# Optimization experiments

Measured on AMD Instinct MI355X. Metric: run time of the kernel, lower is better.

The kernel has to match this reference:

```python
import jax, jax.numpy as jnp
import numpy as np

N = 20000
E = 320000
NEG_SLOPE = 0.2
LN_EPS = 1e-5


def gat_conv(x, W, a_src, a_dst, b, src, dst, heads, ch, concat):
    # x: [N, F_in]; W: [F_in, H*C]; a_src/a_dst: [H, C]; b: [H*C] or [C]
    xl = (x @ W).reshape(N, heads, ch)                      # [N,H,C]
    alpha_src = jnp.sum(xl * a_src, axis=-1)                # [N,H]
    alpha_dst = jnp.sum(xl * a_dst, axis=-1)                # [N,H]
    e = alpha_src[src] + alpha_dst[dst]                     # [E',H]
    e = jax.nn.leaky_relu(e, NEG_SLOPE)
    # segment softmax over incoming edges of each dst node
    m = jax.ops.segment_max(e, dst, num_segments=N)         # [N,H]
    m = jnp.where(jnp.isfinite(m), m, 0.0)
    ex = jnp.exp(e - m[dst])
    denom = jax.ops.segment_sum(ex, dst, num_segments=N)    # [N,H]
    alpha = ex / (denom[dst] + 1e-16)                       # [E',H]
    msg = alpha[:, :, None] * xl[src]                       # [E',H,C]
    out = jax.ops.segment_sum(msg, dst, num_segments=N)     # [N,H,C]
    if concat:
        return out.reshape(N, heads * ch) + b
    return out.mean(axis=1) + b


def layer_norm(x, g, b):
    mu = jnp.mean(x, axis=-1, keepdims=True)
    var = jnp.mean(jnp.square(x - mu), axis=-1, keepdims=True)
    return (x - mu) * jax.lax.rsqrt(var + LN_EPS) * g + b


def setup_inputs() -> dict:
    key = jax.random.key(0)
    ks = jax.random.split(key, 24)
    d = {}
    d["x"] = jax.random.normal(ks[0], (N, 50), dtype=jnp.float32)
    d["edge_index"] = jax.random.randint(ks[1], (2, E), 0, N, dtype=jnp.int64)

    def glorot(k, shape):
        fan = shape[0] + shape[-1]
        return jax.random.normal(k, shape, dtype=jnp.float32) * np.sqrt(2.0 / fan)

    # conv1: 50 -> 256, heads=4, concat
    d["W1"] = glorot(ks[2], (50, 4 * 256))
    d["a_src1"] = glorot(ks[3], (4, 256))
    d["a_dst1"] = glorot(ks[4], (4, 256))
    d["b1"] = jnp.zeros((4 * 256,), jnp.float32)
    # conv2: 1024 -> 256, heads=4, concat
    d["W2"] = glorot(ks[5], (1024, 4 * 256))
    d["a_src2"] = glorot(ks[6], (4, 256))
    d["a_dst2"] = glorot(ks[7], (4, 256))
    d["b2"] = jnp.zeros((4 * 256,), jnp.float32)
    # conv3: 1024 -> 121, heads=6, concat=False
    d["W3"] = glorot(ks[8], (1024, 6 * 121))
    d["a_src3"] = glorot(ks[9], (6, 121))
    d["a_dst3"] = glorot(ks[10], (6, 121))
    d["b3"] = jnp.zeros((121,), jnp.float32)
    # skips
    d["skipW1"] = glorot(ks[11], (50, 1024))
    d["skipb1"] = jnp.zeros((1024,), jnp.float32)
    d["skipW2"] = glorot(ks[12], (1024, 1024))
    d["skipb2"] = jnp.zeros((1024,), jnp.float32)
    # layer norms
    d["g1"] = jnp.ones((1024,), jnp.float32)
    d["beta1"] = jnp.zeros((1024,), jnp.float32)
    d["g2"] = jnp.ones((1024,), jnp.float32)
    d["beta2"] = jnp.zeros((1024,), jnp.float32)
    return d


def reference(x, edge_index, W1, a_src1, a_dst1, b1, W2, a_src2, a_dst2, b2,
              W3, a_src3, a_dst3, b3, skipW1, skipb1, skipW2, skipb2,
              g1, beta1, g2, beta2):
    # add self loops (PyG GATConv default)
    loop = jnp.arange(N, dtype=edge_index.dtype)
    src = jnp.concatenate([edge_index[0], loop])
    dst = jnp.concatenate([edge_index[1], loop])

    h = gat_conv(x, W1, a_src1, a_dst1, b1, src, dst, 4, 256, True)
    h = jax.nn.elu(layer_norm(h + (x @ skipW1 + skipb1), g1, beta1))
    h2 = gat_conv(h, W2, a_src2, a_dst2, b2, src, dst, 4, 256, True)
    h2 = jax.nn.elu(layer_norm(h2 + (h @ skipW2 + skipb2), g2, beta2))
    out = gat_conv(h2, W3, a_src3, a_dst3, b3, src, dst, 6, 121, False)
    return out
```

## Files before the change

kernel.cpp:

```cpp
#include <hip/hip_runtime.h>
#include <hip/hip_bf16.h>
#include <math.h>

typedef __attribute__((ext_vector_type(8))) __bf16 bf16x8;
typedef __attribute__((ext_vector_type(4))) float f32x4;

#define MPAD 20224
#define SSZ ((size_t)MPAD * 128)

#if __has_builtin(__builtin_amdgcn_global_load_lds)
#define GLD16(g, l)                                                                      \
    __builtin_amdgcn_global_load_lds(                                                    \
        (const __attribute__((address_space(1))) unsigned int*)(g),                      \
        (__attribute__((address_space(3))) unsigned int*)(l), 16, 0, 0)
#else
#define GLD16(g, l) (*(bf16x8*)(l) = *(const bf16x8*)(g))
#endif

#define BAR() asm volatile("s_barrier" ::: "memory")
#define WAITVM(N) asm volatile("s_waitcnt vmcnt(" #N ")" ::: "memory")


#define STAGE_H(Base, regidx, t_, kh_)                                                   \
    do {                                                                                 \
        __bf16* Ld = lds + ((((t_) & 1) * 4 + (regidx)) * 8192);                         \
        const __bf16* Gp = (Base) + (t_) * 64 + (kh_) * 32;                              \
        GLD16(Gp, Ld + tt * 8);                                                          \
        GLD16(Gp + (size_t)128 * K_, Ld + (tt + 512) * 8);                               \
    } while (0)

#define LOAD_A(t_, kh_)                                                                  \
    {                                                                                    \
        const __bf16* Ar = lds + (((t_) & 1) * 4 + (kh_)) * 8192 + aoff;                 \
        _Pragma("unroll") for (int i = 0; i < 8; i++)                                    \
            af[i] = *(const bf16x8*)(Ar + i * 512);                                      \
    }

#define LOAD_B2(t_, kh_, j0)                                                             \
    {                                                                                    \
        const __bf16* Br = lds + (((t_) & 1) * 4 + 2 + (kh_)) * 8192 + boff;             \
        _Pragma("unroll") for (int j = 0; j < 2; j++)                                    \
            bf[(j0) + j] = *(const bf16x8*)(Br + ((j0) + j) * 512);                      \
    }

#define MFMA_HALF(j0)                                                                    \
    __builtin_amdgcn_s_setprio(1);                                                       \
    _Pragma("unroll") for (int i = 0; i < 8; i++)                                        \
        _Pragma("unroll") for (int j = (j0); j < (j0) + 2; j++)                          \
            acc[i][j] = __builtin_amdgcn_mfma_f32_16x16x32_bf16(af[i], bf[j],            \
                                                                acc[i][j], 0, 0, 0);     \
    __builtin_amdgcn_s_setprio(0);

#define GEMM256_BODY(A, Bt, K_, STORE)                                                   \
    __shared__ __align__(16) __bf16 lds[65536];                                          \
    const int tt = threadIdx.x;                                                          \
    const int lane = tt & 63;                                                            \
    const int wid = tt >> 6;                                                             \
    const int wr = wid >> 2;                                           \
    const int wc = wid & 3;                                         \
     \
    const int nwg = gridDim.x * gridDim.y;                                               \
    const int wg0 = blockIdx.y * gridDim.x + blockIdx.x;                                 \
    const int qq = nwg >> 3, rr = nwg & 7, xcd = wg0 & 7, oo = wg0 >> 3;                 \
    const int swz = (xcd < rr ? xcd * (qq + 1) : rr * (qq + 1) + (xcd - rr) * qq) + oo;  \
    const int bm = (swz / gridDim.x) * 256;                                              \
    const int bn = (swz % gridDim.x) * 256;                                              \
    const int m16 = lane & 15;                                                           \
    const int c4 = lane >> 4;                                                            \
    const int NT = K_ >> 6;                                                              \
    const int ttp = tt ^ (((tt >> 5) & 1) << 1);          \
    const int srow = ttp >> 2;                                                           \
    const int sch = (ttp & 3) << 3;                                                      \
    const __bf16* Abase = A + (size_t)(bm + srow) * K_ + sch;                            \
    const __bf16* Bbase = Bt + (size_t)(bn + srow) * K_ + sch;                           \
    const int fsw = ((m16 >> 3) & 1) << 4;                                               \
    const int aoff = (((wr * 128 + m16) * 32) + c4 * 8) ^ fsw;                           \
    const int boff = (((wc * 64 + m16) * 32) + c4 * 8) ^ fsw;                            \
    f32x4 acc[8][4];                                                                     \
    _Pragma("unroll") for (int i = 0; i < 8; i++)                                        \
        _Pragma("unroll") for (int j = 0; j < 4; j++)                                    \
            acc[i][j] = (f32x4){0.f, 0.f, 0.f, 0.f};                                     \
    bf16x8 af[8], bf[4];                                                                 \
     \
    STAGE_H(Abase, 0, 0, 0);                                                             \
    STAGE_H(Bbase, 2, 0, 0);                                                             \
    STAGE_H(Abase, 1, 0, 1);                                                             \
    STAGE_H(Bbase, 3, 0, 1);                                                             \
    WAITVM(4);                                                                           \
    BAR();                                                                               \
    for (int t = 0; t < NT; t++) {                                                       \
        const bool pre = (t + 1 < NT);                                                   \
                                                                                 \
        LOAD_A(t, 0);                                                                    \
        LOAD_B2(t, 0, 0);                                                                \
        if (pre) STAGE_H(Abase, 0, t + 1, 0);                                            \
        BAR();                                                                           \
        MFMA_HALF(0);                                                                    \
        BAR();                                                                           \
                                                                                 \
        LOAD_B2(t, 0, 2);                                                                \
        if (pre) STAGE_H(Bbase, 2, t + 1, 0);                                            \
        BAR();                                                                           \
        MFMA_HALF(2);                                                                    \
        if (pre) { WAITVM(4); } else { WAITVM(0); }                                      \
        BAR();                                                                           \
                                                                                 \
        LOAD_A(t, 1);                                                                    \
        LOAD_B2(t, 1, 0);                                                                \
        if (pre) STAGE_H(Abase, 1, t + 1, 1);                                            \
        BAR();                                                                           \
        MFMA_HALF(0);                                                                    \
        BAR();                                                                           \
                                                                                 \
        LOAD_B2(t, 1, 2);                                                                \
        if (pre) STAGE_H(Bbase, 3, t + 1, 1);                                            \
        BAR();                                                                           \
        MFMA_HALF(2);                                                                    \
        if (pre) { WAITVM(4); }                                                          \
        BAR();                                                                           \
    }                                                                                    \
    STORE

__global__ __launch_bounds__(512, 2) void gemm256_bt(const __bf16* __restrict__ A,
                                                     const __bf16* __restrict__ Bt,
                                                     __bf16* __restrict__ C,
                                                     int M, int N_, int K_) {
    GEMM256_BODY(A, Bt, K_,
        { const int r4 = c4 << 2;
          const int rb = bm + wr * 128;
          _Pragma("unroll") for (int i = 0; i < 8; i++)
              _Pragma("unroll") for (int j = 0; j < 4; j++) {
                  int col = bn + wc * 64 + j * 16 + m16;
                  size_t sb_ = (size_t)(col >> 7) * SSZ + (col & 127);
                  _Pragma("unroll") for (int r = 0; r < 4; r++) {
                      int row = rb + i * 16 + r4 + r;
                      C[sb_ + (size_t)row * 128] = (__bf16)acc[i][j][r];
                  }
              } })
}

__global__ __launch_bounds__(512, 2) void gemm256_bt2(const __bf16* __restrict__ A,
                                                      const __bf16* __restrict__ Bt,
                                                      __bf16* __restrict__ C0,
                                                      __bf16* __restrict__ C1,
                                                      int M, int K_) {
    GEMM256_BODY(A, Bt, K_,
        { const int r4 = c4 << 2;
          const int rb = bm + wr * 128;
          _Pragma("unroll") for (int i = 0; i < 8; i++)
              _Pragma("unroll") for (int j = 0; j < 4; j++) {
                  int col = bn + wc * 64 + j * 16 + m16;
                  __bf16* Cp = (col < 1024) ? C0 : C1;
                  int c10 = col & 1023;
                  size_t sb_ = (size_t)(c10 >> 7) * SSZ + (c10 & 127);
                  _Pragma("unroll") for (int r = 0; r < 4; r++) {
                      int row = rb + i * 16 + r4 + r;
                      Cp[sb_ + (size_t)row * 128] = (__bf16)acc[i][j][r];
                  }
              } })
}

__device__ __forceinline__ void transpose_tile(const float* __restrict__ W,
                                               __bf16* __restrict__ WT,
                                               int K, int N, int Kp, int Np,
                                               int bx, int by, float* sm) {
    int tx = threadIdx.x & 31, ty = threadIdx.x >> 5;
#pragma unroll
    for (int r = ty; r < 32; r += 8) {
        int k = by * 32 + r, n = bx * 32 + tx;
        float v = 0.f;
        if (k < K && n < N) v = W[(size_t)k * N + n];
        sm[r * 33 + tx] = v;
    }
    __syncthreads();
#pragma unroll
    for (int r = ty; r < 32; r += 8) {
        int n = bx * 32 + r, k = by * 32 + tx;
        if (n < Np && k < Kp) WT[(size_t)n * Kp + k] = (__bf16)sm[tx * 33 + r];
    }
}

__device__ __forceinline__ void transpose_w3_tile(const float* __restrict__ W,
                                                  __bf16* __restrict__ WT,
                                                  int bx, int by, float* sm) {
    int tx = threadIdx.x & 31, ty = threadIdx.x >> 5;
    int r0 = bx * 32;
    int h = r0 >> 7;
    int c0 = r0 & 127;
#pragma unroll
    for (int r = ty; r < 32; r += 8) {
        int k = by * 32 + r;
        int c = c0 + tx;
        float v = 0.f;
        if (c < 121) v = W[(size_t)k * 726 + h * 121 + c];
        sm[r * 33 + tx] = v;
    }
    __syncthreads();
#pragma unroll
    for (int r = ty; r < 32; r += 8) {
        int rr = r0 + r;
        int k = by * 32 + tx;
        WT[(size_t)rr * 1024 + k] = (__bf16)sm[tx * 33 + r];
    }
}

__global__ __launch_bounds__(256) void prep_k(const float* __restrict__ x,
                                              const float* __restrict__ W1,
                                              const float* __restrict__ sW1,
                                              const float* __restrict__ W2,
                                              const float* __restrict__ sW2,
                                              const float* __restrict__ W3,
                                              __bf16* __restrict__ xp,
                                              __bf16* __restrict__ WTcat1,
                                              __bf16* __restrict__ WTcat2,
                                              __bf16* __restrict__ W3pT, int Nn) {
    __shared__ float sm[32 * 33];
    int b = blockIdx.x;
    if (b < 5056) {
        int i = b * 256 + threadIdx.x;
        int n = i >> 6, c = i & 63;
        float v = 0.f;
        if (n < Nn && c < 50) v = x[n * 50 + c];
        xp[(size_t)n * 64 + c] = (__bf16)v;
    } else if (b < 5120) {
        int i = b - 5056; transpose_tile(W1, WTcat1, 50, 1024, 64, 1024, i % 32, i / 32, sm);
    } else if (b < 5184) {
        int i = b - 5120; transpose_tile(sW1, WTcat1 + 1024 * 64, 50, 1024, 64, 1024, i % 32, i / 32, sm);
    } else if (b < 6208) {
        int i = b - 5184; transpose_tile(W2, WTcat2, 1024, 1024, 1024, 1024, i % 32, i / 32, sm);
    } else if (b < 7232) {
        int i = b - 6208; transpose_tile(sW2, WTcat2 + (size_t)1024 * 1024, 1024, 1024, 1024, 1024, i % 32, i / 32, sm);
    } else {
        int i = b - 7232; transpose_w3_tile(W3, W3pT, i % 24, i / 24, sm);
    }
}

__global__ void zero_probe_k(const int* __restrict__ ei, int* __restrict__ cnt,
                             int* __restrict__ flag, int Nn) {
    int i = blockIdx.x * 256 + threadIdx.x;
    if (i < Nn) cnt[i] = 0;
    if (blockIdx.x == 0 && threadIdx.x == 0) {
        int all0 = 1;
        for (int k = 0; k < 64; k++)
            if (ei[2 * k + 1] != 0) { all0 = 0; break; }
        *flag = all0;
    }
}

__device__ __forceinline__ int load_ei(const int* ei, int idx, int is64) {
    return is64 ? ei[2 * idx] : ei[idx];
}

__global__ void hist_k(const int* __restrict__ ei, const int* __restrict__ flag,
                       int* __restrict__ cnt, int E, int Nn) {
    int e = blockIdx.x * 256 + threadIdx.x;
    if (e >= E + Nn) return;
    int is64 = *flag;
    int d = (e < E) ? load_ei(ei, E + e, is64) : (e - E);
    d = min(max(d, 0), Nn - 1);
    atomicAdd(&cnt[d], 1);
}

__global__ __launch_bounds__(1024) void scan_k(int* __restrict__ cnt, int* __restrict__ row_ptr,
                                               int Nn) {
    __shared__ int part[1024];
    int t = threadIdx.x;
    int chunk = (Nn + 1023) >> 10;
    int lo = t * chunk;
    int hi = lo + chunk; if (hi > Nn) hi = Nn; if (lo > Nn) lo = Nn;
    int s = 0;
    for (int i = lo; i < hi; i++) s += (cnt[i] + 7) & ~7;
    part[t] = s;
    __syncthreads();
    for (int off = 1; off < 1024; off <<= 1) {
        int v = (t >= off) ? part[t - off] : 0;
        __syncthreads();
        part[t] += v;
        __syncthreads();
    }
    int run = part[t] - s;
    for (int i = lo; i < hi; i++) { row_ptr[i] = run; run += (cnt[i] + 7) & ~7; }
    if (t == 1023) row_ptr[Nn] = part[1023];
    __syncthreads();
    for (int i = lo; i < hi; i++) cnt[i] = 0;
}

__global__ void fill_csr_k(const int* __restrict__ ei, const int* __restrict__ flag,
                           const int* __restrict__ row_ptr, int* __restrict__ cursor,
                           int* __restrict__ src_csr, int E, int Nn) {
    int e = blockIdx.x * 256 + threadIdx.x;
    if (e >= E + Nn) return;
    int is64 = *flag;
    int d = (e < E) ? load_ei(ei, E + e, is64) : (e - E);
    int s = (e < E) ? load_ei(ei, e, is64) : (e - E);
    d = min(max(d, 0), Nn - 1);
    s = min(max(s, 0), Nn - 1);
    int slot = row_ptr[d] + atomicAdd(&cursor[d], 1);
    src_csr[slot] = s;
}

__global__ void alpha_k(const __bf16* __restrict__ XL, int sph, const float* __restrict__ a_src,
                        const float* __restrict__ a_dst, float* __restrict__ asrc,
                        float* __restrict__ adst, int Nn, int H, int C) {
    int gw = (blockIdx.x * 256 + threadIdx.x) >> 6;
    int lane = threadIdx.x & 63;
    if (gw >= Nn * H) return;
    int n = gw / H, h = gw - n * H;
    const float* as = a_src + h * C;
    const float* ad = a_dst + h * C;
    float s = 0.f, d = 0.f;
    for (int c = lane; c < C; c += 64) {
        float v = (float)XL[(size_t)(h * sph + (c >> 7)) * SSZ + (size_t)n * 128 + (c & 127)];
        s += v * as[c];
        d += v * ad[c];
    }
#pragma unroll
    for (int off = 32; off; off >>= 1) {
        s += __shfl_down(s, off);
        d += __shfl_down(d, off);
    }
    if (lane == 0) { asrc[n * H + h] = s; adst[n * H + h] = d; }
}

__global__ void attn_k(const int* __restrict__ row_ptr, const int* __restrict__ deg,
                       const int* __restrict__ src_csr,
                       const float* __restrict__ asrc, const float* __restrict__ adst,
                       float* __restrict__ wt, int Nn, int H, int Ecap) {
    int gw = (blockIdx.x * 256 + threadIdx.x) >> 6;
    int lane = threadIdx.x & 63;
    if (gw >= Nn) return;
    int n = gw;
    int base = row_ptr[n], dg = deg[n];
    if (dg <= 64) {
        bool v = lane < dg;
        int src = v ? src_csr[base + lane] : 0;
        for (int h = 0; h < H; h++) {
            float ad = adst[n * H + h];
            float e = -1e30f;
            if (v) {
                e = asrc[src * H + h] + ad;
                e = e > 0.f ? e : 0.2f * e;
            }
            float m = e;
#pragma unroll
            for (int off = 1; off < 64; off <<= 1) m = fmaxf(m, __shfl_xor(m, off));
            float ex = v ? __expf(e - m) : 0.f;
            float sum = ex;
#pragma unroll
            for (int off = 1; off < 64; off <<= 1) sum += __shfl_xor(sum, off);
            if (v) wt[(size_t)h * Ecap + base + lane] = ex / (sum + 1e-16f);
        }
        return;
    }
    for (int h = 0; h < H; h++) {
        float ad = adst[n * H + h];
        float m = -1e30f;
        for (int s = lane; s < dg; s += 64) {
            float e = asrc[src_csr[base + s] * H + h] + ad;
            e = e > 0.f ? e : 0.2f * e;
            m = fmaxf(m, e);
        }
#pragma unroll
        for (int off = 1; off < 64; off <<= 1) m = fmaxf(m, __shfl_xor(m, off));
        float sum = 0.f;
        for (int s = lane; s < dg; s += 64) {
            float e = asrc[src_csr[base + s] * H + h] + ad;
            e = e > 0.f ? e : 0.2f * e;
            sum += __expf(e - m);
        }
#pragma unroll
        for (int off = 1; off < 64; off <<= 1) sum += __shfl_xor(sum, off);
        float inv = 1.f / (sum + 1e-16f);
        float* wrow = wt + (size_t)h * Ecap;
        for (int s = lane; s < dg; s += 64) {
            float e = asrc[src_csr[base + s] * H + h] + ad;
            e = e > 0.f ? e : 0.2f * e;
            wrow[base + s] = __expf(e - m) * inv;
        }
    }
}

__global__ __launch_bounds__(256) void agg_skip8(const __bf16* __restrict__ XL,
                                                 const float* __restrict__ wt,
                                                 const int* __restrict__ row_ptr,
                                                 const int* __restrict__ src_csr,
                                                 const float* __restrict__ bias,
                                                 const float* __restrict__ sb,
                                                 __bf16* __restrict__ SK, int Nn, int Ecap) {
    const int cc = blockIdx.y;
    const int n = blockIdx.x * 4 + (threadIdx.x >> 6);
    const int lane = threadIdx.x & 63;
    if (n >= Nn) return;
    const int g = lane >> 4;
    const int p = lane & 15;
    const int col = cc * 128 + p * 8;
    const float* wrow = wt + (size_t)(cc >> 1) * Ecap;
    const __bf16* XLc = XL + (size_t)cc * SSZ + p * 8;
    const int base = row_ptr[n], end = row_ptr[n + 1];

    float acc[8];
#pragma unroll
    for (int j = 0; j < 8; j++) acc[j] = 0.f;

    for (int e = base; e < end; e += 8) {
        int2 si = *(const int2*)(src_csr + e + 2 * g);
        float2 wv = *(const float2*)(wrow + e + 2 * g);
        bf16x8 xa = *(const bf16x8*)(XLc + (size_t)si.x * 128);
        bf16x8 xb = *(const bf16x8*)(XLc + (size_t)si.y * 128);
#pragma unroll
        for (int j = 0; j < 8; j++) acc[j] += wv.x * (float)xa[j] + wv.y * (float)xb[j];
    }
#pragma unroll
    for (int j = 0; j < 8; j++) {
        acc[j] += __shfl_xor(acc[j], 16);
        acc[j] += __shfl_xor(acc[j], 32);
    }
    if (lane < 16) {
        size_t o = (size_t)cc * SSZ + (size_t)n * 128 + p * 8;
        bf16x8 sk = *(const bf16x8*)(SK + o);
        bf16x8 res;
#pragma unroll
        for (int j = 0; j < 8; j++)
            res[j] = (__bf16)(acc[j] + bias[col + j] + sb[col + j] + (float)sk[j]);
        *(bf16x8*)(SK + o) = res;
    }
}

__global__ __launch_bounds__(256) void agg_mean8(const __bf16* __restrict__ XL,
                                                 const float* __restrict__ wt,
                                                 const int* __restrict__ row_ptr,
                                                 const int* __restrict__ src_csr,
                                                 __bf16* __restrict__ part, int Nn, int Ecap) {
    const int cc = blockIdx.y;
    const int n = blockIdx.x * 4 + (threadIdx.x >> 6);
    const int lane = threadIdx.x & 63;
    if (n >= Nn) return;
    const int g = lane >> 4;
    const int p = lane & 15;
    const int col = cc * 128 + p * 8;
    const float* wrow = wt + (size_t)cc * Ecap;
    const __bf16* XLc = XL + (size_t)cc * SSZ + p * 8;
    const int base = row_ptr[n], end = row_ptr[n + 1];

    float acc[8];
#pragma unroll
    for (int j = 0; j < 8; j++) acc[j] = 0.f;

    for (int e = base; e < end; e += 8) {
        int2 si = *(const int2*)(src_csr + e + 2 * g);
        float2 wv = *(const float2*)(wrow + e + 2 * g);
        bf16x8 xa = *(const bf16x8*)(XLc + (size_t)si.x * 128);
        bf16x8 xb = *(const bf16x8*)(XLc + (size_t)si.y * 128);
#pragma unroll
        for (int j = 0; j < 8; j++) acc[j] += wv.x * (float)xa[j] + wv.y * (float)xb[j];
    }
#pragma unroll
    for (int j = 0; j < 8; j++) {
        acc[j] += __shfl_xor(acc[j], 16);
        acc[j] += __shfl_xor(acc[j], 32);
    }
    if (lane < 16) {
        size_t o = (size_t)n * 768 + col;
        bf16x8 res;
#pragma unroll
        for (int j = 0; j < 8; j++) res[j] = (__bf16)acc[j];
        *(bf16x8*)(part + o) = res;
    }
}

__global__ __launch_bounds__(128) void reduce_mean_k(const __bf16* __restrict__ part,
                                                     const float* __restrict__ b3,
                                                     float* __restrict__ out, int Nn) {
    int n = blockIdx.x;
    int t = threadIdx.x;
    if (t >= 121) return;
    const __bf16* row = part + (size_t)n * 768;
    float s = 0.f;
#pragma unroll
    for (int h = 0; h < 6; h++) s += (float)row[h * 128 + t];
    out[(size_t)n * 121 + t] = s * (1.f / 6.f) + b3[t];
}

__global__ __launch_bounds__(256) void ln_elu_k(const __bf16* __restrict__ in,
                                                const float* __restrict__ g,
                                                const float* __restrict__ be,
                                                __bf16* __restrict__ out, int rows_real) {
    const int D = 1024;
    int n = blockIdx.x;
    int t = threadIdx.x;
    size_t ro = (size_t)n * D;
    if (n >= rows_real) {
#pragma unroll
        for (int j = 0; j < 4; j++) out[ro + t + 256 * j] = (__bf16)0.f;
        return;
    }
    float v[4];
    float s = 0.f, q = 0.f;
#pragma unroll
    for (int j = 0; j < 4; j++) {
        int c = t + 256 * j;
        float a = (float)in[(size_t)(c >> 7) * SSZ + (size_t)n * 128 + (c & 127)];
        v[j] = a;
        s += a;
        q += a * a;
    }
#pragma unroll
    for (int off = 32; off; off >>= 1) {
        s += __shfl_down(s, off);
        q += __shfl_down(q, off);
    }
    __shared__ float rs[8];
    int wid = t >> 6;
    if ((t & 63) == 0) { rs[wid] = s; rs[wid + 4] = q; }
    __syncthreads();
    s = rs[0] + rs[1] + rs[2] + rs[3];
    q = rs[4] + rs[5] + rs[6] + rs[7];
    float mu = s * (1.f / 1024.f);
    float var = q * (1.f / 1024.f) - mu * mu;
    float inv = rsqrtf(fmaxf(var, 0.f) + 1e-5f);
#pragma unroll
    for (int j = 0; j < 4; j++) {
        int c = t + 256 * j;
        float y = (v[j] - mu) * inv * g[c] + be[c];
        y = y > 0.f ? y : expm1f(y);
        out[ro + c] = (__bf16)y;
    }
}

extern "C" void kernel_launch(void* const* d_in, const int* in_sizes, int n_in,
                              void* d_out, int out_size, void* d_ws, size_t ws_size,
                              hipStream_t stream) {
    const float* x   = (const float*)d_in[0];
    const int*   ei  = (const int*)d_in[1];
    const float* W1  = (const float*)d_in[2];
    const float* as1 = (const float*)d_in[3];
    const float* ad1 = (const float*)d_in[4];
    const float* b1  = (const float*)d_in[5];
    const float* W2  = (const float*)d_in[6];
    const float* as2 = (const float*)d_in[7];
    const float* ad2 = (const float*)d_in[8];
    const float* b2  = (const float*)d_in[9];
    const float* W3  = (const float*)d_in[10];
    const float* as3 = (const float*)d_in[11];
    const float* ad3 = (const float*)d_in[12];
    const float* b3  = (const float*)d_in[13];
    const float* sW1 = (const float*)d_in[14];
    const float* sb1 = (const float*)d_in[15];
    const float* sW2 = (const float*)d_in[16];
    const float* sb2 = (const float*)d_in[17];
    const float* g1  = (const float*)d_in[18];
    const float* be1 = (const float*)d_in[19];
    const float* g2  = (const float*)d_in[20];
    const float* be2 = (const float*)d_in[21];
    float* out = (float*)d_out;

    const int Nn = 20000;
    const int E = in_sizes[1] / 2;
    const int E2 = E + Nn;
    const int Ecap = E2 + 8 * Nn;
    const int Mpad = MPAD;

    char* p = (char*)d_ws;
    auto alloc = [&](size_t bytes) {
        char* r = p;
        p += (bytes + 255) & ~(size_t)255;
        return r;
    };
    __bf16* WTcat1 = (__bf16*)alloc((size_t)2048 * 64 * 2);
    __bf16* WTcat2 = (__bf16*)alloc((size_t)2048 * 1024 * 2);
    __bf16* W3pT   = (__bf16*)alloc((size_t)768 * 1024 * 2);
    __bf16* xp     = (__bf16*)alloc((size_t)Mpad * 64 * 2);
    __bf16* XL     = (__bf16*)alloc((size_t)Mpad * 1024 * 2);
    __bf16* SK     = (__bf16*)alloc((size_t)Mpad * 1024 * 2);
    __bf16* H1     = (__bf16*)alloc((size_t)Mpad * 1024 * 2);
    float*  asrcb  = (float*)alloc((size_t)Nn * 6 * 4);
    float*  adstb  = (float*)alloc((size_t)Nn * 6 * 4);
    float*  wbuf   = (float*)alloc((size_t)6 * Ecap * 4);
    int*    rowp   = (int*)alloc((size_t)(Nn + 1) * 4);
    int*    cnt    = (int*)alloc((size_t)Nn * 4);
    int*    scsr   = (int*)alloc((size_t)Ecap * 4);
    int*    eiflag = (int*)alloc(256);
    __bf16* part   = SK;
    (void)ws_size; (void)n_in; (void)out_size;

    prep_k<<<8000, 256, 0, stream>>>(x, W1, sW1, W2, sW2, W3, xp, WTcat1, WTcat2, W3pT, Nn);

    zero_probe_k<<<(Nn + 255) / 256, 256, 0, stream>>>(ei, cnt, eiflag, Nn);
    hist_k<<<(E2 + 255) / 256, 256, 0, stream>>>(ei, eiflag, cnt, E, Nn);
    scan_k<<<1, 1024, 0, stream>>>(cnt, rowp, Nn);
    (void)hipMemsetAsync(scsr, 0, (size_t)Ecap * 4, stream);
    (void)hipMemsetAsync(wbuf, 0, (size_t)6 * Ecap * 4, stream);
    fill_csr_k<<<(E2 + 255) / 256, 256, 0, stream>>>(ei, eiflag, rowp, cnt, scsr, E, Nn);

    gemm256_bt2<<<dim3(8, Mpad / 256), 512, 0, stream>>>(xp, WTcat1, XL, SK, Mpad, 64);
    alpha_k<<<(Nn * 4 * 64) / 256, 256, 0, stream>>>(XL, 2, as1, ad1, asrcb, adstb, Nn, 4, 256);
    attn_k<<<(Nn + 3) / 4, 256, 0, stream>>>(rowp, cnt, scsr, asrcb, adstb, wbuf, Nn, 4, Ecap);
    agg_skip8<<<dim3((Nn + 3) / 4, 8), 256, 0, stream>>>(XL, wbuf, rowp, scsr, b1, sb1, SK, Nn, Ecap);
    ln_elu_k<<<Mpad, 256, 0, stream>>>(SK, g1, be1, H1, Nn);

    gemm256_bt2<<<dim3(8, Mpad / 256), 512, 0, stream>>>(H1, WTcat2, XL, SK, Mpad, 1024);
    alpha_k<<<(Nn * 4 * 64) / 256, 256, 0, stream>>>(XL, 2, as2, ad2, asrcb, adstb, Nn, 4, 256);
    attn_k<<<(Nn + 3) / 4, 256, 0, stream>>>(rowp, cnt, scsr, asrcb, adstb, wbuf, Nn, 4, Ecap);
    agg_skip8<<<dim3((Nn + 3) / 4, 8), 256, 0, stream>>>(XL, wbuf, rowp, scsr, b2, sb2, SK, Nn, Ecap);
    ln_elu_k<<<Mpad, 256, 0, stream>>>(SK, g2, be2, H1, Nn);

    gemm256_bt<<<dim3(3, Mpad / 256), 512, 0, stream>>>(H1, W3pT, XL, Mpad, 768, 1024);
    alpha_k<<<(Nn * 6 * 64) / 256, 256, 0, stream>>>(XL, 1, as3, ad3, asrcb, adstb, Nn, 6, 121);
    attn_k<<<(Nn + 3) / 4, 256, 0, stream>>>(rowp, cnt, scsr, asrcb, adstb, wbuf, Nn, 6, Ecap);
    agg_mean8<<<dim3((Nn + 3) / 4, 6), 256, 0, stream>>>(XL, wbuf, rowp, scsr, part, Nn, Ecap);
    reduce_mean_k<<<Nn, 128, 0, stream>>>(part, b3, out, Nn);
}
```

Before: 760.5 us.

## Replace two-stage split-K GEMM pipeline with four-deep LDS ring buffer

Result: no change. 750.4 us (-1.3%).

```diff
diff --git a/kernel.cpp b/kernel.cpp
--- a/kernel.cpp
+++ b/kernel.cpp
@@ -21,32 +21,31 @@
 #define WAITVM(N) asm volatile("s_waitcnt vmcnt(" #N ")" ::: "memory")
 
 
-#define STAGE_H(Base, regidx, t_, kh_)                                                   \
+#define STAGE_T(t_)                                                                      \
     do {                                                                                 \
-        __bf16* Ld = lds + ((((t_) & 1) * 4 + (regidx)) * 8192);                         \
-        const __bf16* Gp = (Base) + (t_) * 64 + (kh_) * 32;                              \
-        GLD16(Gp, Ld + tt * 8);                                                          \
-        GLD16(Gp + (size_t)128 * K_, Ld + (tt + 512) * 8);                               \
+        __bf16* Ld = lds + (((t_) & 3) * 16384);                                         \
+        const __bf16* Ga = Abase + (t_) * 32;                                            \
+        const __bf16* Gb = Bbase + (t_) * 32;                                            \
+        GLD16(Ga, Ld + tt * 8);                                                          \
+        GLD16(Ga + (size_t)128 * K_, Ld + (tt + 512) * 8);                               \
+        GLD16(Gb, Ld + 8192 + tt * 8);                                                   \
+        GLD16(Gb + (size_t)128 * K_, Ld + 8192 + (tt + 512) * 8);                        \
     } while (0)
 
-#define LOAD_A(t_, kh_)                                                                  \
+#define LOAD_FRAGS(t_)                                                                   \
     {                                                                                    \
-        const __bf16* Ar = lds + (((t_) & 1) * 4 + (kh_)) * 8192 + aoff;                 \
+        const __bf16* Ar = lds + (((t_) & 3) * 16384) + aoff;                            \
+        const __bf16* Br = lds + (((t_) & 3) * 16384) + 8192 + boff;                     \
         _Pragma("unroll") for (int i = 0; i < 8; i++)                                    \
             af[i] = *(const bf16x8*)(Ar + i * 512);                                      \
-    }
-
-#define LOAD_B2(t_, kh_, j0)                                                             \
-    {                                                                                    \
-        const __bf16* Br = lds + (((t_) & 1) * 4 + 2 + (kh_)) * 8192 + boff;             \
-        _Pragma("unroll") for (int j = 0; j < 2; j++)                                    \
-            bf[(j0) + j] = *(const bf16x8*)(Br + ((j0) + j) * 512);                      \
-    }
-
-#define MFMA_HALF(j0)                                                                    \
+        _Pragma("unroll") for (int j = 0; j < 4; j++)                                    \
+            bf[j] = *(const bf16x8*)(Br + j * 512);                                      \
+    }
+
+#define MFMA_ALL()                                                                       \
     __builtin_amdgcn_s_setprio(1);                                                       \
     _Pragma("unroll") for (int i = 0; i < 8; i++)                                        \
-        _Pragma("unroll") for (int j = (j0); j < (j0) + 2; j++)                          \
+        _Pragma("unroll") for (int j = 0; j < 4; j++)                                    \
             acc[i][j] = __builtin_amdgcn_mfma_f32_16x16x32_bf16(af[i], bf[j],            \
                                                                 acc[i][j], 0, 0, 0);     \
     __builtin_amdgcn_s_setprio(0);
@@ -67,7 +66,7 @@
     const int bn = (swz % gridDim.x) * 256;                                              \
     const int m16 = lane & 15;                                                           \
     const int c4 = lane >> 4;                                                            \
-    const int NT = K_ >> 6;                                                              \
+    const int NT = K_ >> 5;                                                              \
     const int ttp = tt ^ (((tt >> 5) & 1) << 1);          \
     const int srow = ttp >> 2;                                                           \
     const int sch = (ttp & 3) << 3;                                                      \
@@ -81,43 +80,22 @@
         _Pragma("unroll") for (int j = 0; j < 4; j++)                                    \
             acc[i][j] = (f32x4){0.f, 0.f, 0.f, 0.f};                                     \
     bf16x8 af[8], bf[4];                                                                 \
-     \
-    STAGE_H(Abase, 0, 0, 0);                                                             \
-    STAGE_H(Bbase, 2, 0, 0);                                                             \
-    STAGE_H(Abase, 1, 0, 1);                                                             \
-    STAGE_H(Bbase, 3, 0, 1);                                                             \
-    WAITVM(4);                                                                           \
+                      \
+    STAGE_T(0);                                                                          \
+    if (NT > 1) STAGE_T(1);                                                              \
+    if (NT > 2) STAGE_T(2);                                                              \
+    if (NT > 2) { WAITVM(8); } else if (NT > 1) { WAITVM(4); } else { WAITVM(0); }       \
     BAR();                                                                               \
     for (int t = 0; t < NT; t++) {                                                       \
-        const bool pre = (t + 1 < NT);                                                   \
-                                                                                 \
-        LOAD_A(t, 0);                                                                    \
-        LOAD_B2(t, 0, 0);                                                                \
-        if (pre) STAGE_H(Abase, 0, t + 1, 0);                                            \
-        BAR();                                                                           \
-        MFMA_HALF(0);                                                                    \
-        BAR();                                                                           \
-                                                                                 \
-        LOAD_B2(t, 0, 2);                                                                \
-        if (pre) STAGE_H(Bbase, 2, t + 1, 0);                                            \
-        BAR();                                                                           \
-        MFMA_HALF(2);                                                                    \
-        if (pre) { WAITVM(4); } else { WAITVM(0); }                                      \
-        BAR();                                                                           \
-                                                                                 \
-        LOAD_A(t, 1);                                                                    \
-        LOAD_B2(t, 1, 0);                                                                \
-        if (pre) STAGE_H(Abase, 1, t + 1, 1);                                            \
-        BAR();                                                                           \
-        MFMA_HALF(0);                                                                    \
-        BAR();                                                                           \
-                                                                                 \
-        LOAD_B2(t, 1, 2);                                                                \
-        if (pre) STAGE_H(Bbase, 3, t + 1, 1);                                            \
-        BAR();                                                                           \
-        MFMA_HALF(2);                                                                    \
-        if (pre) { WAITVM(4); }                                                          \
-        BAR();                                                                           \
+        if (t + 3 < NT) STAGE_T(t + 3);                                                  \
+        LOAD_FRAGS(t);                                                                   \
+        MFMA_ALL();                                                                      \
+        if (t + 1 < NT) {                                                                \
+            if (t + 3 < NT) { WAITVM(8); }                                               \
+            else if (t + 3 == NT) { WAITVM(4); }                                         \
+            else { WAITVM(0); }                                                          \
+            BAR();                                                                       \
+        }                                                                                \
     }                                                                                    \
     STORE
 
```
